# Performance work log

Measured on AMD Instinct MI355X. Metric: run time of the kernel, lower is better.

## Reference

```python
import jax, jax.numpy as jnp
import numpy as np
from jax import ops

NEG_SLOPE = 0.2
EPS = 1e-5


def layer_norm(v, g, b):
    mu = jnp.mean(v, axis=-1, keepdims=True)
    var = jnp.mean(jnp.square(v - mu), axis=-1, keepdims=True)
    return (v - mu) * jax.lax.rsqrt(var + EPS) * g + b


def gat_conv(x, src, dst, W, a_src, a_dst, bias, N, H, C, concat):
    # linear projection, per-head view [N, H, C]
    h = (x @ W).reshape(N, H, C)
    alpha_src = jnp.sum(h * a_src, axis=-1)  # [N, H]
    alpha_dst = jnp.sum(h * a_dst, axis=-1)  # [N, H]
    # per-edge raw attention logits [E, H]
    e = alpha_src[src] + alpha_dst[dst]
    e = jnp.where(e > 0, e, NEG_SLOPE * e)  # leaky relu
    # segment softmax over destination node
    m = ops.segment_max(e, dst, num_segments=N)  # [N, H]
    a = jnp.exp(e - m[dst])
    s = ops.segment_sum(a, dst, num_segments=N)  # [N, H]
    a = a / s[dst]
    # weighted scatter-aggregate: [E, H, C] messages -> [N, H, C]
    out = ops.segment_sum(h[src] * a[:, :, None], dst, num_segments=N)
    if concat:
        return out.reshape(N, H * C) + bias
    return jnp.mean(out, axis=1) + bias


def setup_inputs() -> dict:
    key = jax.random.key(0)
    ks = jax.random.split(key, 16)
    N, E, IN, H, C1, C2 = 50000, 800000, 128, 4, 64, 64
    sd_in = 1.0 / np.sqrt(IN)
    sd_h = 1.0 / np.sqrt(H * C1)
    return {
        "x": jax.random.normal(ks[0], (N, IN), jnp.float32),
        "edge_index": jax.random.randint(ks[1], (2, E), 0, N, jnp.int64),
        # GAT layer 1 (in -> H*C1, concat)
        "W1": jax.random.normal(ks[2], (IN, H * C1), jnp.float32) * sd_in,
        "att_src1": jax.random.normal(ks[3], (H, C1), jnp.float32) * sd_in,
        "att_dst1": jax.random.normal(ks[4], (H, C1), jnp.float32) * sd_in,
        "bias1": jnp.zeros((H * C1,), jnp.float32),
        "g1": jnp.ones((H * C1,), jnp.float32),
        "b1": jnp.zeros((H * C1,), jnp.float32),
        # GAT layer 2 (H*C1 -> C2, mean over heads)
        "W2": jax.random.normal(ks[5], (H * C1, H * C2), jnp.float32) * sd_h,
        "att_src2": jax.random.normal(ks[6], (H, C2), jnp.float32) * sd_h,
        "att_dst2": jax.random.normal(ks[7], (H, C2), jnp.float32) * sd_h,
        "bias2": jnp.zeros((C2,), jnp.float32),
        "g2": jnp.ones((C2,), jnp.float32),
        "b2": jnp.zeros((C2,), jnp.float32),
        # residual projection (in != out)
        "Wres": jax.random.normal(ks[8], (IN, C2), jnp.float32) * sd_in,
        "bres": jnp.zeros((C2,), jnp.float32),
    }


def reference(x, edge_index, W1, att_src1, att_dst1, bias1, g1, b1,
              W2, att_src2, att_dst2, bias2, g2, b2, Wres, bres):
    N = x.shape[0]
    H, C1 = att_src1.shape
    C2 = att_src2.shape[1]
    # PyG GATConv add_self_loops=True
    loop = jnp.arange(N, dtype=edge_index.dtype)
    src = jnp.concatenate([edge_index[0], loop])
    dst = jnp.concatenate([edge_index[1], loop])

    identity = x @ Wres + bres
    h1 = gat_conv(x, src, dst, W1, att_src1, att_dst1, bias1, N, H, C1, concat=True)
    h1 = jax.nn.elu(layer_norm(h1, g1, b1))  # dropout inactive (eval)
    h2 = gat_conv(h1, src, dst, W2, att_src2, att_dst2, bias2, N, H, C2, concat=False)
    h2 = layer_norm(h2, g2, b2)
    return jax.nn.elu(h2 + identity)
```

## Files before the change

### kernel.cpp

```cpp
#include <hip/hip_runtime.h>
#include <math.h>

#define HH 4
#define CC 64
#define HC 256
#define CAP 96

static constexpr float NEG_SLOPE = 0.2f;
static constexpr float LN_EPS = 1e-5f;

typedef __attribute__((ext_vector_type(8))) short short8;
typedef __attribute__((ext_vector_type(4))) float floatx4;
typedef __attribute__((ext_vector_type(4))) unsigned int uintx4;

__device__ __forceinline__ float bf2f(unsigned short u) {
  return __uint_as_float(((unsigned int)u) << 16);
}
__device__ __forceinline__ unsigned short f2bf(float f) {
  unsigned int u = __float_as_uint(f);
  u = (u + 0x7fff + ((u >> 16) & 1)) >> 16;
  return (unsigned short)u;
}
__device__ __forceinline__ unsigned int pack2bf(float a, float b) {
  return (unsigned int)f2bf(a) | ((unsigned int)f2bf(b) << 16);
}

__device__ __forceinline__ void macc8(float* acc, uintx4 h, float w) {
  acc[0] += w * __uint_as_float(h.x << 16);
  acc[1] += w * __uint_as_float(h.x & 0xffff0000u);
  acc[2] += w * __uint_as_float(h.y << 16);
  acc[3] += w * __uint_as_float(h.y & 0xffff0000u);
  acc[4] += w * __uint_as_float(h.z << 16);
  acc[5] += w * __uint_as_float(h.z & 0xffff0000u);
  acc[6] += w * __uint_as_float(h.w << 16);
  acc[7] += w * __uint_as_float(h.w & 0xffff0000u);
}

__device__ __forceinline__ short8 ldA8(const unsigned short* A, size_t idx) {
  return *(const short8*)(A + idx);
}
__device__ __forceinline__ short8 ldA8(const float* A, size_t idx) {
  const float4 u = *(const float4*)(A + idx);
  const float4 v = *(const float4*)(A + idx + 4);
  short8 r;
  r[0] = (short)f2bf(u.x); r[1] = (short)f2bf(u.y);
  r[2] = (short)f2bf(u.z); r[3] = (short)f2bf(u.w);
  r[4] = (short)f2bf(v.x); r[5] = (short)f2bf(v.y);
  r[6] = (short)f2bf(v.z); r[7] = (short)f2bf(v.w);
  return r;
}

__global__ __launch_bounds__(256) void prep_kernel(
    const float* __restrict__ W1, const float* __restrict__ W2,
    const float* __restrict__ Wres,
    unsigned short* __restrict__ wt1c, unsigned short* __restrict__ wt2,
    int* __restrict__ deg, int N) {
  const int idx = blockIdx.x * 256 + threadIdx.x;
  if (idx < 49152) {
    const int r = idx >> 7, k = idx & 127;
    float v = 0.f;
    if (r < 256) v = W1[k * 256 + r];
    else if (r < 320) v = Wres[k * 64 + (r - 256)];
    wt1c[idx] = f2bf(v);
  } else if (idx < 49152 + 65536) {
    const int i = idx - 49152;
    const int r = i >> 8, k = i & 255;
    wt2[i] = f2bf(W2[k * 256 + r]);
  } else if (idx < 49152 + 65536 + N) {
    deg[idx - 49152 - 65536] = 0;
  }
}

template <typename AT>
__global__ __launch_bounds__(256) void gemm128(
    const AT* __restrict__ A, const unsigned short* __restrict__ BT,
    unsigned short* __restrict__ Chm,
    float* __restrict__ ident, const float* __restrict__ bres,
    const float* __restrict__ att_src, const float* __restrict__ att_dst,
    float* __restrict__ as_, float* __restrict__ ad_,
    int M, int K, int GM,
    const int* __restrict__ srcs, const int* __restrict__ dsts,
    int* __restrict__ deg, int* __restrict__ col, int E, int N, int S) {
  const int bid = blockIdx.x;
  const int tid = threadIdx.x;
  int gid = bid;
  if (S > 0) {
    const int q = bid / 3;
    const bool is_scatter = (bid % 3 == 2) && (q < S);
    if (is_scatter) {
      const int base = q * 4096 + tid * 16;
#pragma unroll
      for (int k = 0; k < 16; ++k) {
        const int e = base + k;
        if (e < E + N) {
          int s, d;
          if (e < E) { s = srcs[e]; d = dsts[e]; }
          else       { s = e - E; d = s; }
          const int pos = atomicAdd(&deg[d], 1);
          col[d * CAP + pos] = s;
        }
      }
      return;
    }
    gid = bid - (q < S ? q : S);
  }
  const int bx = gid % GM, by = gid / GM;

  __shared__ unsigned short As[128][40];
  __shared__ unsigned short Bs[128][40];
  const int w = tid >> 6, lane = tid & 63;
  const int q4 = lane >> 4, mr = lane & 15;
  const int rh = w >> 1, ch = w & 1;
  const int row0 = bx * 128;
  const int col0 = by * 128;
  const int sr = tid >> 2;
  const int sk = (tid & 3) * 8;

  floatx4 acc[4][4] = {};

  short8 a0 = {}, a1 = {}, b0, b1;
  {
    const int r0 = row0 + sr, r1 = row0 + sr + 64;
    if (r0 < M) a0 = ldA8(A, (size_t)r0 * K + sk);
    if (r1 < M) a1 = ldA8(A, (size_t)r1 * K + sk);
    b0 = *(const short8*)(BT + (size_t)(col0 + sr) * K + sk);
    b1 = *(const short8*)(BT + (size_t)(col0 + sr + 64) * K + sk);
  }
  for (int k0 = 0; k0 < K; k0 += 32) {
    *(short8*)(&As[sr][sk]) = a0;
    *(short8*)(&As[sr + 64][sk]) = a1;
    *(short8*)(&Bs[sr][sk]) = b0;
    *(short8*)(&Bs[sr + 64][sk]) = b1;
    __syncthreads();
    const int kn = k0 + 32;
    if (kn < K) {
      const int r0 = row0 + sr, r1 = row0 + sr + 64;
      a0 = (r0 < M) ? ldA8(A, (size_t)r0 * K + kn + sk) : short8{};
      a1 = (r1 < M) ? ldA8(A, (size_t)r1 * K + kn + sk) : short8{};
      b0 = *(const short8*)(BT + (size_t)(col0 + sr) * K + kn + sk);
      b1 = *(const short8*)(BT + (size_t)(col0 + sr + 64) * K + kn + sk);
    }
    short8 af[4], bf[4];
#pragma unroll
    for (int i = 0; i < 4; ++i)
      af[i] = *(const short8*)(&As[rh * 64 + i * 16 + mr][q4 * 8]);
#pragma unroll
    for (int j = 0; j < 4; ++j)
      bf[j] = *(const short8*)(&Bs[ch * 64 + j * 16 + mr][q4 * 8]);
#pragma unroll
    for (int i = 0; i < 4; ++i)
#pragma unroll
      for (int j = 0; j < 4; ++j)
        acc[i][j] = __builtin_amdgcn_mfma_f32_16x16x32_bf16(af[i], bf[j], acc[i][j], 0, 0, 0);
    __syncthreads();
  }
  if (col0 < 256) {
    const int hh = (col0 >> 6) + ch;
#pragma unroll
    for (int i = 0; i < 4; ++i)
#pragma unroll
      for (int j = 0; j < 4; ++j)
#pragma unroll
        for (int rr = 0; rr < 4; ++rr) {
          const int row = row0 + rh * 64 + i * 16 + q4 * 4 + rr;
          if (row < M)
            Chm[((size_t)hh * M + row) * 64 + j * 16 + mr] = f2bf(acc[i][j][rr]);
        }
    float pa[16] = {}, pb[16] = {};
#pragma unroll
    for (int j = 0; j < 4; ++j) {
      const float a_s = att_src[hh * 64 + j * 16 + mr];
      const float a_d = att_dst[hh * 64 + j * 16 + mr];
#pragma unroll
      for (int i = 0; i < 4; ++i)
#pragma unroll
        for (int rr = 0; rr < 4; ++rr) {
          pa[i * 4 + rr] += acc[i][j][rr] * a_s;
          pb[i * 4 + rr] += acc[i][j][rr] * a_d;
        }
    }
#pragma unroll
    for (int off = 1; off < 16; off <<= 1) {
#pragma unroll
      for (int t = 0; t < 16; ++t) {
        pa[t] += __shfl_xor(pa[t], off);
        pb[t] += __shfl_xor(pb[t], off);
      }
    }
    if (mr == 0) {
#pragma unroll
      for (int i = 0; i < 4; ++i)
#pragma unroll
        for (int rr = 0; rr < 4; ++rr) {
          const int row = row0 + rh * 64 + i * 16 + q4 * 4 + rr;
          if (row < M) {
            as_[row * 4 + hh] = pa[i * 4 + rr];
            ad_[row * 4 + hh] = pb[i * 4 + rr];
          }
        }
    }
  } else if (ch == 0) {
#pragma unroll
    for (int i = 0; i < 4; ++i)
#pragma unroll
      for (int j = 0; j < 4; ++j)
#pragma unroll
        for (int rr = 0; rr < 4; ++rr) {
          const int row = row0 + rh * 64 + i * 16 + q4 * 4 + rr;
          if (row < M) {
            const int cc = j * 16 + mr;
            ident[(size_t)row * 64 + cc] = acc[i][j][rr] + bres[cc];
          }
        }
  }
}

__global__ __launch_bounds__(512) void gemm256(
    const unsigned short* __restrict__ A, const unsigned short* __restrict__ BT,
    unsigned short* __restrict__ Chm,
    const float* __restrict__ att_src, const float* __restrict__ att_dst,
    float* __restrict__ as_, float* __restrict__ ad_, int M, int K) {
  __shared__ unsigned short As[128][40];
  __shared__ unsigned short Bs[256][40];
  const int tid = threadIdx.x;
  const int w = tid >> 6, lane = tid & 63;
  const int q4 = lane >> 4, mr = lane & 15;
  const int rh = w >> 2, ch = w & 3;
  const int row0 = blockIdx.x * 128;
  const int sr = tid >> 2;
  const int sk = (tid & 3) * 8;

  floatx4 acc[4][4] = {};
  short8 a0 = {}, b0, b1;
  {
    const int r0 = row0 + sr;
    if (r0 < M) a0 = ldA8(A, (size_t)r0 * K + sk);
    b0 = *(const short8*)(BT + (size_t)sr * K + sk);
    b1 = *(const short8*)(BT + (size_t)(sr + 128) * K + sk);
  }
  for (int k0 = 0; k0 < K; k0 += 32) {
    *(short8*)(&As[sr][sk]) = a0;
    *(short8*)(&Bs[sr][sk]) = b0;
    *(short8*)(&Bs[sr + 128][sk]) = b1;
    __syncthreads();
    const int kn = k0 + 32;
    if (kn < K) {
      const int r0 = row0 + sr;
      a0 = (r0 < M) ? ldA8(A, (size_t)r0 * K + kn + sk) : short8{};
      b0 = *(const short8*)(BT + (size_t)sr * K + kn + sk);
      b1 = *(const short8*)(BT + (size_t)(sr + 128) * K + kn + sk);
    }
    short8 af[4], bf[4];
#pragma unroll
    for (int i = 0; i < 4; ++i)
      af[i] = *(const short8*)(&As[rh * 64 + i * 16 + mr][q4 * 8]);
#pragma unroll
    for (int j = 0; j < 4; ++j)
      bf[j] = *(const short8*)(&Bs[ch * 64 + j * 16 + mr][q4 * 8]);
#pragma unroll
    for (int i = 0; i < 4; ++i)
#pragma unroll
      for (int j = 0; j < 4; ++j)
        acc[i][j] = __builtin_amdgcn_mfma_f32_16x16x32_bf16(af[i], bf[j], acc[i][j], 0, 0, 0);
    __syncthreads();
  }
  const int hh = ch;
#pragma unroll
  for (int i = 0; i < 4; ++i)
#pragma unroll
    for (int j = 0; j < 4; ++j)
#pragma unroll
      for (int rr = 0; rr < 4; ++rr) {
        const int row = row0 + rh * 64 + i * 16 + q4 * 4 + rr;
        if (row < M)
          Chm[((size_t)hh * M + row) * 64 + j * 16 + mr] = f2bf(acc[i][j][rr]);
      }
  float pa[16] = {}, pb[16] = {};
#pragma unroll
  for (int j = 0; j < 4; ++j) {
    const float a_s = att_src[hh * 64 + j * 16 + mr];
    const float a_d = att_dst[hh * 64 + j * 16 + mr];
#pragma unroll
    for (int i = 0; i < 4; ++i)
#pragma unroll
      for (int rr = 0; rr < 4; ++rr) {
        pa[i * 4 + rr] += acc[i][j][rr] * a_s;
        pb[i * 4 + rr] += acc[i][j][rr] * a_d;
      }
  }
#pragma unroll
  for (int off = 1; off < 16; off <<= 1) {
#pragma unroll
    for (int t = 0; t < 16; ++t) {
      pa[t] += __shfl_xor(pa[t], off);
      pb[t] += __shfl_xor(pb[t], off);
    }
  }
  if (mr == 0) {
#pragma unroll
    for (int i = 0; i < 4; ++i)
#pragma unroll
      for (int rr = 0; rr < 4; ++rr) {
        const int row = row0 + rh * 64 + i * 16 + q4 * 4 + rr;
        if (row < M) {
          as_[row * 4 + hh] = pa[i * 4 + rr];
          ad_[row * 4 + hh] = pb[i * 4 + rr];
        }
      }
  }
}

__global__ __launch_bounds__(256) void agg_gather(
    const int* __restrict__ deg, const int* __restrict__ col,
    const float* __restrict__ as_, const float* __restrict__ ad_,
    const unsigned short* __restrict__ hlin_hm,
    unsigned short* __restrict__ agg, int N) {
  const int b = blockIdx.x;
  const int hh = b & 3;
  const int w = threadIdx.x >> 6, lane = threadIdx.x & 63;
  const int g = lane >> 4;
  const int sub = (lane >> 3) & 1;
  const int cg = lane & 7;
  const int el = lane & 15;
  const int gb = lane & 48;
  const int n = (b >> 3) * 32 + ((b >> 2) & 1) * 16 + w * 4 + g;
  const bool valid = n < N;
  const int n_c = valid ? n : 0;
  const uintx4* hb = (const uintx4*)(hlin_hm + (size_t)hh * N * 64) + cg;
  const float adv = ad_[n_c * 4 + hh];
  const int cnt = valid ? deg[n_c] : 0;
  const int* cbase = col + n_c * CAP;
  float acc[8] = {};
  float wsum = 0.f;
  for (int off = 0;; off += 16) {
    const int len = cnt - off;
    int lm = len > 16 ? 16 : (len < 0 ? 0 : len);
    lm = max(lm, __shfl_xor(lm, 16));
    lm = max(lm, __shfl_xor(lm, 32));
    if (lm == 0) break;
    int s_l = 0;
    float w_l = 0.f;
    if (el < len) {
      s_l = cbase[off + el];
      float v = as_[s_l * 4 + hh] + adv;
      v = v > 0.f ? v : NEG_SLOPE * v;
      w_l = __expf(v);
    }
    wsum += w_l;
    int j = 0;
    for (; j + 4 <= lm; j += 4) {
      const int sA = __shfl(s_l, gb + j + sub);
      const int sB = __shfl(s_l, gb + j + 2 + sub);
      const float wA = __shfl(w_l, gb + j + sub);
      const float wB = __shfl(w_l, gb + j + 2 + sub);
      const uintx4 hA = hb[(size_t)sA * 8];
      const uintx4 hB = hb[(size_t)sB * 8];
      macc8(acc, hA, wA);
      macc8(acc, hB, wB);
    }
    for (; j < lm; j += 2) {
      const int s = __shfl(s_l, gb + j + sub);
      const float wt = __shfl(w_l, gb + j + sub);
      macc8(acc, hb[(size_t)s * 8], wt);
    }
  }
  wsum += __shfl_xor(wsum, 1);
  wsum += __shfl_xor(wsum, 2);
  wsum += __shfl_xor(wsum, 4);
  wsum += __shfl_xor(wsum, 8);
#pragma unroll
  for (int t = 0; t < 8; ++t) acc[t] += __shfl_xor(acc[t], 8);
  if (sub == 0 && valid) {
    const float inv = 1.0f / wsum;
    uintx4 o;
    o.x = pack2bf(acc[0] * inv, acc[1] * inv);
    o.y = pack2bf(acc[2] * inv, acc[3] * inv);
    o.z = pack2bf(acc[4] * inv, acc[5] * inv);
    o.w = pack2bf(acc[6] * inv, acc[7] * inv);
    ((uintx4*)(agg + ((size_t)hh * N + n) * 64))[cg] = o;
  }
}

__global__ __launch_bounds__(256) void combine_ln1(
    const unsigned short* __restrict__ agg, const float* __restrict__ bias1,
    const float* __restrict__ g1, const float* __restrict__ b1,
    unsigned short* __restrict__ h1, int N) {
  const int n = blockIdx.x;
  const int tid = threadIdx.x;
  const int hh = tid >> 6, lane = tid & 63;
  const float val = bf2f(agg[((size_t)hh * N + n) * 64 + lane]) + bias1[tid];
  float s1 = val, s2 = val * val;
#pragma unroll
  for (int off = 32; off > 0; off >>= 1) {
    s1 += __shfl_down(s1, off);
    s2 += __shfl_down(s2, off);
  }
  __shared__ float ws1[4], ws2[4];
  if (lane == 0) { ws1[hh] = s1; ws2[hh] = s2; }
  __syncthreads();
  const float tot1 = ws1[0] + ws1[1] + ws1[2] + ws1[3];
  const float tot2 = ws2[0] + ws2[1] + ws2[2] + ws2[3];
  const float mu = tot1 * (1.0f / HC);
  const float var = tot2 * (1.0f / HC) - mu * mu;
  float y = (val - mu) * rsqrtf(var + LN_EPS) * g1[tid] + b1[tid];
  y = y > 0.f ? y : expm1f(y);
  h1[(size_t)n * HC + tid] = f2bf(y);
}

__global__ __launch_bounds__(256) void combine_final(
    const unsigned short* __restrict__ agg, const float* __restrict__ ident,
    const float* __restrict__ bias2, const float* __restrict__ g2,
    const float* __restrict__ b2, float* __restrict__ out, int N) {
  const int n = blockIdx.x * 4 + (threadIdx.x >> 6);
  const int c = threadIdx.x & 63;
  if (n >= N) return;
  float v = 0.25f * (bf2f(agg[((size_t)0 * N + n) * 64 + c]) +
                     bf2f(agg[((size_t)1 * N + n) * 64 + c]) +
                     bf2f(agg[((size_t)2 * N + n) * 64 + c]) +
                     bf2f(agg[((size_t)3 * N + n) * 64 + c])) +
            bias2[c];
  float s1 = v, s2 = v * v;
#pragma unroll
  for (int off = 32; off > 0; off >>= 1) {
    s1 += __shfl_down(s1, off);
    s2 += __shfl_down(s2, off);
  }
  s1 = __shfl(s1, 0);
  s2 = __shfl(s2, 0);
  const float mu = s1 * (1.0f / 64.0f);
  const float var = s2 * (1.0f / 64.0f) - mu * mu;
  float y = (v - mu) * rsqrtf(var + LN_EPS) * g2[c] + b2[c];
  y += ident[(size_t)n * 64 + c];
  out[(size_t)n * 64 + c] = y > 0.f ? y : expm1f(y);
}

extern "C" void kernel_launch(void* const* d_in, const int* in_sizes, int n_in,
                              void* d_out, int out_size, void* d_ws, size_t ws_size,
                              hipStream_t stream) {
  const float* x        = (const float*)d_in[0];
  const int*   ei       = (const int*)d_in[1];
  const float* W1       = (const float*)d_in[2];
  const float* att_src1 = (const float*)d_in[3];
  const float* att_dst1 = (const float*)d_in[4];
  const float* bias1    = (const float*)d_in[5];
  const float* g1       = (const float*)d_in[6];
  const float* b1       = (const float*)d_in[7];
  const float* W2       = (const float*)d_in[8];
  const float* att_src2 = (const float*)d_in[9];
  const float* att_dst2 = (const float*)d_in[10];
  const float* bias2    = (const float*)d_in[11];
  const float* g2       = (const float*)d_in[12];
  const float* b2       = (const float*)d_in[13];
  const float* Wres     = (const float*)d_in[14];
  const float* bres     = (const float*)d_in[15];

  const int N = in_sizes[0] / 128;
  const int E = in_sizes[1] / 2;
  const int IN = 128;

  const int* srcs = ei;
  const int* dsts = ei + E;

  char* p = (char*)d_ws;
  auto alloc = [&](size_t bytes) {
    char* r = p;
    p += (bytes + 255) & ~(size_t)255;
    return r;
  };
  float* ident  = (float*)alloc((size_t)N * 64 * 4);
  float* as_    = (float*)alloc((size_t)N * HH * 4);
  float* ad_    = (float*)alloc((size_t)N * HH * 4);
  int* deg      = (int*)alloc((size_t)N * 4);
  int* col      = (int*)alloc((size_t)N * CAP * 4);
  unsigned short* hlin_hm = (unsigned short*)alloc((size_t)N * HC * 2);
  unsigned short* h1b     = (unsigned short*)alloc((size_t)N * HC * 2);
  unsigned short* aggb    = (unsigned short*)alloc((size_t)4 * N * 64 * 2);
  unsigned short* wt1c = (unsigned short*)alloc((size_t)384 * IN * 2);
  unsigned short* wt2  = (unsigned short*)alloc((size_t)HC * HC * 2);

  const int m128 = (N + 127) / 128;
  const int prep_items = 49152 + 65536 + N;
  const int gatherblocks = ((N + 31) / 32) * 8;
  const int G1 = m128 * 3;
  const int S  = (E + N + 4095) / 4096;
  dim3 blk(256);

  prep_kernel<<<(prep_items + 255) / 256, blk, 0, stream>>>(
      W1, W2, Wres, wt1c, wt2, deg, N);

  gemm128<float><<<G1 + S, blk, 0, stream>>>(
      x, wt1c, hlin_hm, ident, bres, att_src1, att_dst1, as_, ad_, N, IN, m128,
      srcs, dsts, deg, col, E, N, S);
  agg_gather<<<gatherblocks, blk, 0, stream>>>(deg, col, as_, ad_, hlin_hm, aggb, N);
  combine_ln1<<<N, blk, 0, stream>>>(aggb, bias1, g1, b1, h1b, N);

  gemm256<<<m128, dim3(512), 0, stream>>>(
      h1b, wt2, hlin_hm, att_src2, att_dst2, as_, ad_, N, HC);
  agg_gather<<<gatherblocks, blk, 0, stream>>>(deg, col, as_, ad_, hlin_hm, aggb, N);
  combine_final<<<(N + 3) / 4, blk, 0, stream>>>(aggb, ident, bias2, g2, b2,
                                                 (float*)d_out, N);
}
```

Before: 329.3 us.

## Fuse aggregation with layernorm epilogues using node-major layout and implicit self-loops

Switches the projected features from head-major to node-major layout so one wave can gather all four heads of a node. The per-head aggregation, the layernorm/ELU combine of layer 1, and the head-mean/layernorm/residual combine of layer 2 now run in one kernel, which removes the intermediate bf16 aggregate buffer and two launches. Self-loops are handled inline instead of being scattered into the adjacency list, so there are fewer atomics and edges. In exchange, each wave now owns a single node rather than four, which lowers per-wave parallelism and makes load balance depend on each node's degree.

After: 336.9 us. 2.3% more time.

```diff
diff --git a/kernel.cpp b/kernel.cpp
--- a/kernel.cpp
+++ b/kernel.cpp
@@ -80,7 +80,7 @@
     float* __restrict__ as_, float* __restrict__ ad_,
     int M, int K, int GM,
     const int* __restrict__ srcs, const int* __restrict__ dsts,
-    int* __restrict__ deg, int* __restrict__ col, int E, int N, int S) {
+    int* __restrict__ deg, int* __restrict__ col, int E, int S) {
   const int bid = blockIdx.x;
   const int tid = threadIdx.x;
   int gid = bid;
@@ -92,10 +92,8 @@
 #pragma unroll
       for (int k = 0; k < 16; ++k) {
         const int e = base + k;
-        if (e < E + N) {
-          int s, d;
-          if (e < E) { s = srcs[e]; d = dsts[e]; }
-          else       { s = e - E; d = s; }
+        if (e < E) {
+          const int s = srcs[e], d = dsts[e];
           const int pos = atomicAdd(&deg[d], 1);
           col[d * CAP + pos] = s;
         }
@@ -164,7 +162,7 @@
         for (int rr = 0; rr < 4; ++rr) {
           const int row = row0 + rh * 64 + i * 16 + q4 * 4 + rr;
           if (row < M)
-            Chm[((size_t)hh * M + row) * 64 + j * 16 + mr] = f2bf(acc[i][j][rr]);
+            Chm[((size_t)row * 4 + hh) * 64 + j * 16 + mr] = f2bf(acc[i][j][rr]);
         }
     float pa[16] = {}, pb[16] = {};
 #pragma unroll
@@ -273,7 +271,7 @@
       for (int rr = 0; rr < 4; ++rr) {
         const int row = row0 + rh * 64 + i * 16 + q4 * 4 + rr;
         if (row < M)
-          Chm[((size_t)hh * M + row) * 64 + j * 16 + mr] = f2bf(acc[i][j][rr]);
+          Chm[((size_t)row * 4 + hh) * 64 + j * 16 + mr] = f2bf(acc[i][j][rr]);
       }
   float pa[16] = {}, pb[16] = {};
 #pragma unroll
@@ -310,39 +308,41 @@
   }
 }
 
-__global__ __launch_bounds__(256) void agg_gather(
+template <int EPI>
+__global__ __launch_bounds__(256) void agg_fused(
     const int* __restrict__ deg, const int* __restrict__ col,
     const float* __restrict__ as_, const float* __restrict__ ad_,
-    const unsigned short* __restrict__ hlin_hm,
-    unsigned short* __restrict__ agg, int N) {
-  const int b = blockIdx.x;
-  const int hh = b & 3;
+    const unsigned short* __restrict__ hlin,
+    const float* __restrict__ pb, const float* __restrict__ pg,
+    const float* __restrict__ pbb, const float* __restrict__ ident,
+    unsigned short* __restrict__ h1, float* __restrict__ out, int N) {
   const int w = threadIdx.x >> 6, lane = threadIdx.x & 63;
   const int g = lane >> 4;
   const int sub = (lane >> 3) & 1;
   const int cg = lane & 7;
   const int el = lane & 15;
   const int gb = lane & 48;
-  const int n = (b >> 3) * 32 + ((b >> 2) & 1) * 16 + w * 4 + g;
-  const bool valid = n < N;
-  const int n_c = valid ? n : 0;
-  const uintx4* hb = (const uintx4*)(hlin_hm + (size_t)hh * N * 64) + cg;
-  const float adv = ad_[n_c * 4 + hh];
-  const int cnt = valid ? deg[n_c] : 0;
-  const int* cbase = col + n_c * CAP;
+  const int n = blockIdx.x * 4 + w;
+  if (n >= N) return;
+  const uintx4* hb = (const uintx4*)hlin + g * 8 + cg;
+  const float adv = ad_[n * 4 + g];
+  float vs = as_[n * 4 + g] + adv;
+  vs = vs > 0.f ? vs : NEG_SLOPE * vs;
+  const float wself = __expf(vs);
   float acc[8] = {};
-  float wsum = 0.f;
-  for (int off = 0;; off += 16) {
+  float wsum = (el == 0) ? wself : 0.f;
+  if (sub == 0) macc8(acc, hb[(size_t)n * 32], wself);
+
+  const int cnt = deg[n];
+  const int* cbase = col + n * CAP;
+  for (int off = 0; off < cnt; off += 16) {
     const int len = cnt - off;
-    int lm = len > 16 ? 16 : (len < 0 ? 0 : len);
-    lm = max(lm, __shfl_xor(lm, 16));
-    lm = max(lm, __shfl_xor(lm, 32));
-    if (lm == 0) break;
+    const int lm = len > 16 ? 16 : len;
     int s_l = 0;
     float w_l = 0.f;
-    if (el < len) {
+    if (el < lm) {
       s_l = cbase[off + el];
-      float v = as_[s_l * 4 + hh] + adv;
+      float v = as_[s_l * 4 + g] + adv;
       v = v > 0.f ? v : NEG_SLOPE * v;
       w_l = __expf(v);
     }
@@ -353,15 +353,15 @@
       const int sB = __shfl(s_l, gb + j + 2 + sub);
       const float wA = __shfl(w_l, gb + j + sub);
       const float wB = __shfl(w_l, gb + j + 2 + sub);
-      const uintx4 hA = hb[(size_t)sA * 8];
-      const uintx4 hB = hb[(size_t)sB * 8];
+      const uintx4 hA = hb[(size_t)sA * 32];
+      const uintx4 hB = hb[(size_t)sB * 32];
       macc8(acc, hA, wA);
       macc8(acc, hB, wB);
     }
     for (; j < lm; j += 2) {
       const int s = __shfl(s_l, gb + j + sub);
       const float wt = __shfl(w_l, gb + j + sub);
-      macc8(acc, hb[(size_t)s * 8], wt);
+      macc8(acc, hb[(size_t)s * 32], wt);
     }
   }
   wsum += __shfl_xor(wsum, 1);
@@ -370,68 +370,79 @@
   wsum += __shfl_xor(wsum, 8);
 #pragma unroll
   for (int t = 0; t < 8; ++t) acc[t] += __shfl_xor(acc[t], 8);
-  if (sub == 0 && valid) {
-    const float inv = 1.0f / wsum;
-    uintx4 o;
-    o.x = pack2bf(acc[0] * inv, acc[1] * inv);
-    o.y = pack2bf(acc[2] * inv, acc[3] * inv);
-    o.z = pack2bf(acc[4] * inv, acc[5] * inv);
-    o.w = pack2bf(acc[6] * inv, acc[7] * inv);
-    ((uintx4*)(agg + ((size_t)hh * N + n) * 64))[cg] = o;
-  }
-}
-
-__global__ __launch_bounds__(256) void combine_ln1(
-    const unsigned short* __restrict__ agg, const float* __restrict__ bias1,
-    const float* __restrict__ g1, const float* __restrict__ b1,
-    unsigned short* __restrict__ h1, int N) {
-  const int n = blockIdx.x;
-  const int tid = threadIdx.x;
-  const int hh = tid >> 6, lane = tid & 63;
-  const float val = bf2f(agg[((size_t)hh * N + n) * 64 + lane]) + bias1[tid];
-  float s1 = val, s2 = val * val;
-#pragma unroll
-  for (int off = 32; off > 0; off >>= 1) {
-    s1 += __shfl_down(s1, off);
-    s2 += __shfl_down(s2, off);
-  }
-  __shared__ float ws1[4], ws2[4];
-  if (lane == 0) { ws1[hh] = s1; ws2[hh] = s2; }
-  __syncthreads();
-  const float tot1 = ws1[0] + ws1[1] + ws1[2] + ws1[3];
-  const float tot2 = ws2[0] + ws2[1] + ws2[2] + ws2[3];
-  const float mu = tot1 * (1.0f / HC);
-  const float var = tot2 * (1.0f / HC) - mu * mu;
-  float y = (val - mu) * rsqrtf(var + LN_EPS) * g1[tid] + b1[tid];
-  y = y > 0.f ? y : expm1f(y);
-  h1[(size_t)n * HC + tid] = f2bf(y);
-}
-
-__global__ __launch_bounds__(256) void combine_final(
-    const unsigned short* __restrict__ agg, const float* __restrict__ ident,
-    const float* __restrict__ bias2, const float* __restrict__ g2,
-    const float* __restrict__ b2, float* __restrict__ out, int N) {
-  const int n = blockIdx.x * 4 + (threadIdx.x >> 6);
-  const int c = threadIdx.x & 63;
-  if (n >= N) return;
-  float v = 0.25f * (bf2f(agg[((size_t)0 * N + n) * 64 + c]) +
-                     bf2f(agg[((size_t)1 * N + n) * 64 + c]) +
-                     bf2f(agg[((size_t)2 * N + n) * 64 + c]) +
-                     bf2f(agg[((size_t)3 * N + n) * 64 + c])) +
-            bias2[c];
-  float s1 = v, s2 = v * v;
-#pragma unroll
-  for (int off = 32; off > 0; off >>= 1) {
-    s1 += __shfl_down(s1, off);
-    s2 += __shfl_down(s2, off);
-  }
-  s1 = __shfl(s1, 0);
-  s2 = __shfl(s2, 0);
-  const float mu = s1 * (1.0f / 64.0f);
-  const float var = s2 * (1.0f / 64.0f) - mu * mu;
-  float y = (v - mu) * rsqrtf(var + LN_EPS) * g2[c] + b2[c];
-  y += ident[(size_t)n * 64 + c];
-  out[(size_t)n * 64 + c] = y > 0.f ? y : expm1f(y);
+  const float inv = 1.0f / wsum;
+
+  if (EPI == 1) {
+    const int cidx = g * 64 + cg * 8;
+    float v[8];
+    float s1 = 0.f, s2 = 0.f;
+#pragma unroll
+    for (int t = 0; t < 8; ++t) {
+      v[t] = acc[t] * inv + pb[cidx + t];
+      s1 += v[t];
+      s2 += v[t] * v[t];
+    }
+#pragma unroll
+    for (int o = 1; o < 64; o <<= 1) {
+      s1 += __shfl_xor(s1, o);
+      s2 += __shfl_xor(s2, o);
+    }
+    const float mu = s1 * (1.0f / 512.0f);
+    const float var = s2 * (1.0f / 512.0f) - mu * mu;
+    const float rs = rsqrtf(var + LN_EPS);
+    if (sub == 0) {
+      float y[8];
+#pragma unroll
+      for (int t = 0; t < 8; ++t) {
+        float yy = (v[t] - mu) * rs * pg[cidx + t] + pbb[cidx + t];
+        y[t] = yy > 0.f ? yy : expm1f(yy);
+      }
+      uintx4 o4;
+      o4.x = pack2bf(y[0], y[1]);
+      o4.y = pack2bf(y[2], y[3]);
+      o4.z = pack2bf(y[4], y[5]);
+      o4.w = pack2bf(y[6], y[7]);
+      *(uintx4*)(h1 + (size_t)n * HC + cidx) = o4;
+    }
+  } else {
+    float v[8];
+#pragma unroll
+    for (int t = 0; t < 8; ++t) v[t] = acc[t] * inv;
+#pragma unroll
+    for (int t = 0; t < 8; ++t) {
+      v[t] += __shfl_xor(v[t], 16);
+      v[t] += __shfl_xor(v[t], 32);
+      v[t] = v[t] * 0.25f + pb[cg * 8 + t];
+    }
+    float s1 = 0.f, s2 = 0.f;
+#pragma unroll
+    for (int t = 0; t < 8; ++t) {
+      s1 += v[t];
+      s2 += v[t] * v[t];
+    }
+#pragma unroll
+    for (int o = 1; o < 8; o <<= 1) {
+      s1 += __shfl_xor(s1, o);
+      s2 += __shfl_xor(s2, o);
+    }
+    const float mu = s1 * (1.0f / 64.0f);
+    const float var = s2 * (1.0f / 64.0f) - mu * mu;
+    const float rs = rsqrtf(var + LN_EPS);
+    if (lane < 8) {
+      const int c0 = cg * 8;
+      const float* idp = ident + (size_t)n * 64 + c0;
+      float y[8];
+#pragma unroll
+      for (int t = 0; t < 8; ++t) {
+        float yy = (v[t] - mu) * rs * pg[c0 + t] + pbb[c0 + t] + idp[t];
+        y[t] = yy > 0.f ? yy : expm1f(yy);
+      }
+      float4 o1 = {y[0], y[1], y[2], y[3]};
+      float4 o2 = {y[4], y[5], y[6], y[7]};
+      *(float4*)(out + (size_t)n * 64 + c0) = o1;
+      *(float4*)(out + (size_t)n * 64 + c0 + 4) = o2;
+    }
+  }
 }
 
 extern "C" void kernel_launch(void* const* d_in, const int* in_sizes, int n_in,
@@ -472,31 +483,29 @@
   float* ad_    = (float*)alloc((size_t)N * HH * 4);
   int* deg      = (int*)alloc((size_t)N * 4);
   int* col      = (int*)alloc((size_t)N * CAP * 4);
-  unsigned short* hlin_hm = (unsigned short*)alloc((size_t)N * HC * 2);
-  unsigned short* h1b     = (unsigned short*)alloc((size_t)N * HC * 2);
-  unsigned short* aggb    = (unsigned short*)alloc((size_t)4 * N * 64 * 2);
+  unsigned short* hlin = (unsigned short*)alloc((size_t)N * HC * 2);
+  unsigned short* h1b  = (unsigned short*)alloc((size_t)N * HC * 2);
   unsigned short* wt1c = (unsigned short*)alloc((size_t)384 * IN * 2);
   unsigned short* wt2  = (unsigned short*)alloc((size_t)HC * HC * 2);
 
   const int m128 = (N + 127) / 128;
   const int prep_items = 49152 + 65536 + N;
-  const int gatherblocks = ((N + 31) / 32) * 8;
+  const int gatherblocks = (N + 3) / 4;
   const int G1 = m128 * 3;
-  const int S  = (E + N + 4095) / 4096;
+  const int S  = (E + 4095) / 4096;
   dim3 blk(256);
 
   prep_kernel<<<(prep_items + 255) / 256, blk, 0, stream>>>(
       W1, W2, Wres, wt1c, wt2, deg, N);
 
   gemm128<float><<<G1 + S, blk, 0, stream>>>(
-      x, wt1c, hlin_hm, ident, bres, att_src1, att_dst1, as_, ad_, N, IN, m128,
-      srcs, dsts, deg, col, E, N, S);
-  agg_gather<<<gatherblocks, blk, 0, stream>>>(deg, col, as_, ad_, hlin_hm, aggb, N);
-  combine_ln1<<<N, blk, 0, stream>>>(aggb, bias1, g1, b1, h1b, N);
+      x, wt1c, hlin, ident, bres, att_src1, att_dst1, as_, ad_, N, IN, m128,
+      srcs, dsts, deg, col, E, S);
+  agg_fused<1><<<gatherblocks, blk, 0, stream>>>(
+      deg, col, as_, ad_, hlin, bias1, g1, b1, nullptr, h1b, nullptr, N);
 
   gemm256<<<m128, dim3(512), 0, stream>>>(
-      h1b, wt2, hlin_hm, att_src2, att_dst2, as_, ad_, N, HC);
-  agg_gather<<<gatherblocks, blk, 0, stream>>>(deg, col, as_, ad_, hlin_hm, aggb, N);
-  combine_final<<<(N + 3) / 4, blk, 0, stream>>>(aggb, ident, bias2, g2, b2,
-                                                 (float*)d_out, N);
-}
+      h1b, wt2, hlin, att_src2, att_dst2, as_, ad_, N, HC);
+  agg_fused<2><<<gatherblocks, blk, 0, stream>>>(
+      deg, col, as_, ad_, hlin, bias2, g2, b2, ident, nullptr, (float*)d_out, N);
+}
```
